# Performance work log

Hardware: AMD Instinct MI355X
Metric: run time of the kernel (lower is better)

Reference implementation:

```python
import jax, jax.numpy as jnp
import numpy as np

ALPHA = 1.0  # init alpha


def setup_inputs() -> dict:
    key = jax.random.key(0)
    X = jax.random.normal(key, (4096, 512), dtype=jnp.float32)
    return {"X": X}


def reference(X):
    # Pairwise squared L2 distances via GEMM expansion:
    # ||x_i - x_j||^2 = ||x_i||^2 + ||x_j||^2 - 2 x_i . x_j
    # (same math as ((X[None]-X[:,None])**2).sum(-1) without the O(N^2 D) blow-up)
    sq = jnp.sum(X * X, axis=1)                      # [N]
    d2 = sq[:, None] + sq[None, :] - 2.0 * (X @ X.T)  # [N, N]
    # track_running_stats=True: sigma^2 = alpha * mean(d2), detached in torch
    sigma_square = ALPHA * jax.lax.stop_gradient(jnp.mean(d2))
    return jnp.exp(-d2 / (2.0 * sigma_square))
```

## Files before the change

kernel.cpp:

```cpp
#include <hip/hip_runtime.h>
#include <cstdint>

typedef unsigned short u16;
typedef unsigned int u32;
typedef __bf16 bf16x8 __attribute__((ext_vector_type(8)));
typedef float f32x4 __attribute__((ext_vector_type(4)));

#define N_ROWS 4096
#define D_COLS 512

__device__ __forceinline__ u16 f2bf(float f) {
    u32 u = __float_as_uint(f);
    u += 0x7fffu + ((u >> 16) & 1u);
    return (u16)(u >> 16);
}

#define GLDS(g, l)                                                            \
    __builtin_amdgcn_global_load_lds(                                         \
        (const __attribute__((address_space(1))) void*)(g),                   \
        (__attribute__((address_space(3))) void*)(l), 16, 0, 0)

__global__ __launch_bounds__(256) void k_prep(const float* __restrict__ X,
                                              u16* __restrict__ Xb,
                                              float* __restrict__ sq,
                                              float* __restrict__ partial) {
    __shared__ float cs[4][512];
    const int tid = threadIdx.x;
    const int w = tid >> 6, l = tid & 63;
    const int row0 = blockIdx.x * 16 + w * 4;
    float csum[8] = {0.f,0.f,0.f,0.f,0.f,0.f,0.f,0.f};
#pragma unroll
    for (int r = 0; r < 4; ++r) {
        const int row = row0 + r;
        const float4* src = (const float4*)(X + (size_t)row * D_COLS);
        float4 f0 = src[l * 2];
        float4 f1 = src[l * 2 + 1];
        float v[8] = {f0.x, f0.y, f0.z, f0.w, f1.x, f1.y, f1.z, f1.w};
        float ss = 0.f;
#pragma unroll
        for (int j = 0; j < 8; ++j) { ss += v[j] * v[j]; csum[j] += v[j]; }
        uint4 st;
        st.x = (u32)f2bf(v[0]) | ((u32)f2bf(v[1]) << 16);
        st.y = (u32)f2bf(v[2]) | ((u32)f2bf(v[3]) << 16);
        st.z = (u32)f2bf(v[4]) | ((u32)f2bf(v[5]) << 16);
        st.w = (u32)f2bf(v[6]) | ((u32)f2bf(v[7]) << 16);
        *(uint4*)(Xb + (size_t)row * D_COLS + l * 8) = st;
#pragma unroll
        for (int m = 32; m > 0; m >>= 1) ss += __shfl_xor(ss, m, 64);
        if (l == 0) sq[row] = ss;
    }
#pragma unroll
    for (int j = 0; j < 8; ++j) cs[w][l * 8 + j] = csum[j];
    __syncthreads();
    for (int d = tid; d < 512; d += 256)
        partial[blockIdx.x * 512 + d] = cs[0][d] + cs[1][d] + cs[2][d] + cs[3][d];
}

__global__ __launch_bounds__(256) void k_sigma(const float* __restrict__ sq,
                                               const float* __restrict__ partial,
                                               float* __restrict__ parts) {
    __shared__ float csm[4][64];
    __shared__ float red[8];
    const int g = blockIdx.x;
    const int t = threadIdx.x;
    const int c = g * 64 + (t & 63);
    const int ch = t >> 6;
    float cssum = 0.f;
#pragma unroll 8
    for (int b = ch * 64; b < ch * 64 + 64; ++b) cssum += partial[b * 512 + c];
    csm[ch][t & 63] = cssum;
    float s1 = sq[g * 512 + t] + sq[g * 512 + 256 + t];
    __syncthreads();
    float s2 = 0.f;
    if (t < 64) {
        float v = csm[0][t] + csm[1][t] + csm[2][t] + csm[3][t];
        s2 = v * v;
    }
#pragma unroll
    for (int m = 32; m > 0; m >>= 1) {
        s1 += __shfl_xor(s1, m, 64);
        s2 += __shfl_xor(s2, m, 64);
    }
    if ((t & 63) == 0) { red[ch] = s1; red[4 + ch] = s2; }
    __syncthreads();
    if (t == 0) {
        parts[g] = red[0] + red[1] + red[2] + red[3];
        parts[8 + g] = red[4];
    }
}

__global__ __launch_bounds__(512, 2) void k_gemm(const u16* __restrict__ Xb,
                                                 const float* __restrict__ sq,
                                                 const float* __restrict__ parts,
                                                 float* __restrict__ out) {
    __shared__ __align__(16) u16 As[3][256 * 32];
    __shared__ __align__(16) u16 Bs[3][256 * 32];
    __shared__ float sqA[256], sqB[256];
    __shared__ float c_sh;

    const int tid = threadIdx.x;
    const int lane = tid & 63;
    const int wid = tid >> 6;
    const int wr = wid >> 2, wc = wid & 3;

    const int bid = blockIdx.x;
    const int xcd = bid & 7, rr = bid >> 3;
    const int by = (xcd >> 2) * 8 + (rr & 7);
    const int bx = (xcd & 3) * 4 + (rr >> 3);
    const int i0 = by * 256, j0 = bx * 256;

    if (tid < 256) sqA[tid] = sq[i0 + tid];
    else           sqB[tid - 256] = sq[j0 + tid - 256];
    if (tid == 0) {
        float S1 = 0.f, S2 = 0.f;
#pragma unroll
        for (int i = 0; i < 8; ++i) { S1 += parts[i]; S2 += parts[8 + i]; }
        const float mean_d2 = 2.f * S1 / (float)N_ROWS
                            - 2.f * S2 / ((float)N_ROWS * (float)N_ROWS);
        c_sh = -1.4426950408889634f / (2.f * mean_d2);
    }

    const int srow = tid >> 2;
    const int sby = (tid & 3) * 16;
    const int ssw = sby ^ ((srow & 3) << 4);
    const char* xb = (const char*)Xb;
    const char* gA0 = xb + (size_t)(i0 + srow) * 1024 + ssw;
    const char* gA1 = xb + (size_t)(i0 + srow + 128) * 1024 + ssw;
    const char* gB0 = xb + (size_t)(j0 + srow) * 1024 + ssw;
    const char* gB1 = xb + (size_t)(j0 + srow + 128) * 1024 + ssw;

#define STAGE(buf, kt)                                                        \
    do {                                                                      \
        GLDS(gA0 + (kt) * 64, (char*)As[buf] + tid * 16);                     \
        GLDS(gA1 + (kt) * 64, (char*)As[buf] + 8192 + tid * 16);              \
        GLDS(gB0 + (kt) * 64, (char*)Bs[buf] + tid * 16);                     \
        GLDS(gB1 + (kt) * 64, (char*)Bs[buf] + 8192 + tid * 16);              \
    } while (0)

    f32x4 acc[8][4];
#pragma unroll
    for (int m = 0; m < 8; ++m)
#pragma unroll
        for (int n = 0; n < 4; ++n) acc[m][n] = (f32x4){0.f, 0.f, 0.f, 0.f};

    const int frow = lane & 15;
    const int klane = lane >> 4;
    const int asw = (klane * 16) ^ ((frow & 3) << 4);
    const int abase = (wr * 128 + frow) * 64 + asw;
    const int bbase = (wc * 64 + frow) * 64 + asw;

    STAGE(0, 0);
    STAGE(1, 1);

    int cb = 0, nb = 2;
    for (int kt = 0; kt < 16; ++kt) {
        if (kt < 15) asm volatile("s_waitcnt vmcnt(4)" ::: "memory");
        else         asm volatile("s_waitcnt vmcnt(0)" ::: "memory");
        asm volatile("s_barrier" ::: "memory");
        if (kt + 2 < 16) STAGE(nb, kt + 2);
        const char* Ab = (const char*)As[cb];
        const char* Bb = (const char*)Bs[cb];
        bf16x8 a[8], b[4];
#pragma unroll
        for (int m = 0; m < 8; ++m) a[m] = *(const bf16x8*)(Ab + abase + m * 1024);
#pragma unroll
        for (int n = 0; n < 4; ++n) b[n] = *(const bf16x8*)(Bb + bbase + n * 1024);
        __builtin_amdgcn_s_setprio(1);
#pragma unroll
        for (int m = 0; m < 8; ++m)
#pragma unroll
            for (int n = 0; n < 4; ++n)
                acc[m][n] = __builtin_amdgcn_mfma_f32_16x16x32_bf16(
                    a[m], b[n], acc[m][n], 0, 0, 0);
        __builtin_amdgcn_s_setprio(0);
        cb = (cb == 2) ? 0 : cb + 1;
        nb = (nb == 2) ? 0 : nb + 1;
    }
#undef STAGE

    const float cval = c_sh;
    const int q = lane >> 4;
#pragma unroll
    for (int m = 0; m < 8; ++m) {
#pragma unroll
        for (int n = 0; n < 4; ++n) {
            const int col = wc * 64 + n * 16 + frow;
            const float sb = sqB[col];
#pragma unroll
            for (int r = 0; r < 4; ++r) {
                const int row = wr * 128 + m * 16 + q * 4 + r;
                const float d2 = sqA[row] + sb - 2.0f * acc[m][n][r];
                out[(size_t)(i0 + row) * N_ROWS + (j0 + col)] = exp2f(cval * d2);
            }
        }
    }
}

extern "C" void kernel_launch(void* const* d_in, const int* in_sizes, int n_in,
                              void* d_out, int out_size, void* d_ws, size_t ws_size,
                              hipStream_t stream) {
    const float* X = (const float*)d_in[0];
    float* out = (float*)d_out;
    char* ws = (char*)d_ws;

    u16*   Xb   = (u16*)ws;
    float* part = (float*)(ws + (4u << 20));
    float* sq   = (float*)(ws + (4u << 20) + (512u << 10));
    float* prt  = (float*)(ws + (4u << 20) + (512u << 10) + (16u << 10));

    hipLaunchKernelGGL(k_prep, dim3(256), dim3(256), 0, stream, X, Xb, sq, part);
    hipLaunchKernelGGL(k_sigma, dim3(8), dim3(256), 0, stream, sq, part, prt);
    hipLaunchKernelGGL(k_gemm, dim3(256), dim3(512), 0, stream, Xb, sq, prt, out);
}
```

Before: 45.83 us.

## Shrink GEMM tile to 128x128 with 4 waves and nontemporal output stores

Changes the fused distance/exp GEMM from 256x256 tiles with 8 waves to 128x128 tiles with 4 waves, launching 1024 blocks with a new XCD-aware block mapping and a revised LDS swizzle. The intent is more blocks per CU and better load balance across CUs. Output stores also become nontemporal to avoid polluting cache with the 64MB result. Smaller tiles cost operand reuse and double global/L2 traffic for the bf16 input.

```diff
diff --git a/kernel.cpp b/kernel.cpp
--- a/kernel.cpp
+++ b/kernel.cpp
@@ -89,28 +89,28 @@
     }
 }
 
-__global__ __launch_bounds__(512, 2) void k_gemm(const u16* __restrict__ Xb,
+__global__ __launch_bounds__(256, 3) void k_gemm(const u16* __restrict__ Xb,
                                                  const float* __restrict__ sq,
                                                  const float* __restrict__ parts,
                                                  float* __restrict__ out) {
-    __shared__ __align__(16) u16 As[3][256 * 32];
-    __shared__ __align__(16) u16 Bs[3][256 * 32];
-    __shared__ float sqA[256], sqB[256];
+    __shared__ __align__(16) u16 As[3][128 * 32];
+    __shared__ __align__(16) u16 Bs[3][128 * 32];
+    __shared__ float sqA[128], sqB[128];
     __shared__ float c_sh;
 
     const int tid = threadIdx.x;
     const int lane = tid & 63;
     const int wid = tid >> 6;
-    const int wr = wid >> 2, wc = wid & 3;
+    const int wr = wid >> 1, wc = wid & 1;
 
     const int bid = blockIdx.x;
     const int xcd = bid & 7, rr = bid >> 3;
-    const int by = (xcd >> 2) * 8 + (rr & 7);
-    const int bx = (xcd & 3) * 4 + (rr >> 3);
-    const int i0 = by * 256, j0 = bx * 256;
-
-    if (tid < 256) sqA[tid] = sq[i0 + tid];
-    else           sqB[tid - 256] = sq[j0 + tid - 256];
+    const int by = (xcd >> 2) * 16 + (rr & 15);
+    const int bx = (xcd & 3) * 8 + (rr >> 4);
+    const int i0 = by * 128, j0 = bx * 128;
+
+    if (tid < 128) sqA[tid] = sq[i0 + tid];
+    else           sqB[tid - 128] = sq[j0 + tid - 128];
     if (tid == 0) {
         float S1 = 0.f, S2 = 0.f;
 #pragma unroll
@@ -120,34 +120,32 @@
         c_sh = -1.4426950408889634f / (2.f * mean_d2);
     }
 
-    const int srow = tid >> 2;
+    const int sr = tid >> 2;
     const int sby = (tid & 3) * 16;
-    const int ssw = sby ^ ((srow & 3) << 4);
+    const int sw0 = sby ^ (((sr >> 1) & 3) << 4);
+    const int sw1 = sby ^ ((((sr + 64) >> 1) & 3) << 4);
     const char* xb = (const char*)Xb;
-    const char* gA0 = xb + (size_t)(i0 + srow) * 1024 + ssw;
-    const char* gA1 = xb + (size_t)(i0 + srow + 128) * 1024 + ssw;
-    const char* gB0 = xb + (size_t)(j0 + srow) * 1024 + ssw;
-    const char* gB1 = xb + (size_t)(j0 + srow + 128) * 1024 + ssw;
+    const char* gA0 = xb + (size_t)(i0 + sr) * 1024 + sw0;
+    const char* gA1 = xb + (size_t)(i0 + sr + 64) * 1024 + sw1;
+    const char* gB0 = xb + (size_t)(j0 + sr) * 1024 + sw0;
+    const char* gB1 = xb + (size_t)(j0 + sr + 64) * 1024 + sw1;
 
 #define STAGE(buf, kt)                                                        \
     do {                                                                      \
         GLDS(gA0 + (kt) * 64, (char*)As[buf] + tid * 16);                     \
-        GLDS(gA1 + (kt) * 64, (char*)As[buf] + 8192 + tid * 16);              \
+        GLDS(gA1 + (kt) * 64, (char*)As[buf] + 4096 + tid * 16);              \
         GLDS(gB0 + (kt) * 64, (char*)Bs[buf] + tid * 16);                     \
-        GLDS(gB1 + (kt) * 64, (char*)Bs[buf] + 8192 + tid * 16);              \
+        GLDS(gB1 + (kt) * 64, (char*)Bs[buf] + 4096 + tid * 16);              \
     } while (0)
 
-    f32x4 acc[8][4];
-#pragma unroll
-    for (int m = 0; m < 8; ++m)
+    f32x4 acc[4][4];
+#pragma unroll
+    for (int m = 0; m < 4; ++m)
 #pragma unroll
         for (int n = 0; n < 4; ++n) acc[m][n] = (f32x4){0.f, 0.f, 0.f, 0.f};
 
     const int frow = lane & 15;
     const int klane = lane >> 4;
-    const int asw = (klane * 16) ^ ((frow & 3) << 4);
-    const int abase = (wr * 128 + frow) * 64 + asw;
-    const int bbase = (wc * 64 + frow) * 64 + asw;
 
     STAGE(0, 0);
     STAGE(1, 1);
@@ -160,14 +158,22 @@
         if (kt + 2 < 16) STAGE(nb, kt + 2);
         const char* Ab = (const char*)As[cb];
         const char* Bb = (const char*)Bs[cb];
-        bf16x8 a[8], b[4];
-#pragma unroll
-        for (int m = 0; m < 8; ++m) a[m] = *(const bf16x8*)(Ab + abase + m * 1024);
-#pragma unroll
-        for (int n = 0; n < 4; ++n) b[n] = *(const bf16x8*)(Bb + bbase + n * 1024);
+        bf16x8 a[4], b[4];
+#pragma unroll
+        for (int m = 0; m < 4; ++m) {
+            const int row = wr * 64 + m * 16 + frow;
+            a[m] = *(const bf16x8*)(Ab + row * 64 +
+                                    ((klane * 16) ^ (((row >> 1) & 3) << 4)));
+        }
+#pragma unroll
+        for (int n = 0; n < 4; ++n) {
+            const int row = wc * 64 + n * 16 + frow;
+            b[n] = *(const bf16x8*)(Bb + row * 64 +
+                                    ((klane * 16) ^ (((row >> 1) & 3) << 4)));
+        }
         __builtin_amdgcn_s_setprio(1);
 #pragma unroll
-        for (int m = 0; m < 8; ++m)
+        for (int m = 0; m < 4; ++m)
 #pragma unroll
             for (int n = 0; n < 4; ++n)
                 acc[m][n] = __builtin_amdgcn_mfma_f32_16x16x32_bf16(
@@ -181,16 +187,18 @@
     const float cval = c_sh;
     const int q = lane >> 4;
 #pragma unroll
-    for (int m = 0; m < 8; ++m) {
+    for (int m = 0; m < 4; ++m) {
 #pragma unroll
         for (int n = 0; n < 4; ++n) {
             const int col = wc * 64 + n * 16 + frow;
             const float sb = sqB[col];
 #pragma unroll
             for (int r = 0; r < 4; ++r) {
-                const int row = wr * 128 + m * 16 + q * 4 + r;
+                const int row = wr * 64 + m * 16 + q * 4 + r;
                 const float d2 = sqA[row] + sb - 2.0f * acc[m][n][r];
-                out[(size_t)(i0 + row) * N_ROWS + (j0 + col)] = exp2f(cval * d2);
+                __builtin_nontemporal_store(
+                    exp2f(cval * d2),
+                    &out[(size_t)(i0 + row) * N_ROWS + (j0 + col)]);
             }
         }
     }
@@ -210,5 +218,5 @@
 
     hipLaunchKernelGGL(k_prep, dim3(256), dim3(256), 0, stream, X, Xb, sq, part);
     hipLaunchKernelGGL(k_sigma, dim3(8), dim3(256), 0, stream, sq, part, prt);
-    hipLaunchKernelGGL(k_gemm, dim3(256), dim3(512), 0, stream, Xb, sq, prt, out);
-}
+    hipLaunchKernelGGL(k_gemm, dim3(1024), dim3(256), 0, stream, Xb, sq, prt, out);
+}
```

New measurement: 53.38 us. 16.5% more time.

## Restructure GEMM main loop into double-buffered BK=64 with interleaved load/MFMA phases

Applied to the files above, without the earlier changes.

Changes the LDS tiling from a triple-buffered 32-wide K step to a double-buffered 64-wide K step with an 8-way XOR swizzle. Each K iteration is split into four phases that interleave partial LDS fragment reads, issues of the next tile's global-to-LDS loads, and MFMA bursts, separated by barriers and explicit waitcnts. The goal is better overlap of memory traffic with matrix math, fewer loop iterations and fewer bank conflicts. The cost is more barriers per iteration and tight vmcnt bookkeeping, which could stall or race if the counts are wrong.

```diff
diff --git a/kernel.cpp b/kernel.cpp
--- a/kernel.cpp
+++ b/kernel.cpp
@@ -89,12 +89,18 @@
     }
 }
 
+#define BAR __builtin_amdgcn_s_barrier()
+#define LGKM0 do { asm volatile("s_waitcnt lgkmcnt(0)" ::: "memory");         \
+                   __builtin_amdgcn_sched_barrier(0); } while (0)
+#define PRIO1 __builtin_amdgcn_s_setprio(1)
+#define PRIO0 __builtin_amdgcn_s_setprio(0)
+
 __global__ __launch_bounds__(512, 2) void k_gemm(const u16* __restrict__ Xb,
                                                  const float* __restrict__ sq,
                                                  const float* __restrict__ parts,
                                                  float* __restrict__ out) {
-    __shared__ __align__(16) u16 As[3][256 * 32];
-    __shared__ __align__(16) u16 Bs[3][256 * 32];
+    __shared__ __align__(16) u16 As[2][256 * 64];
+    __shared__ __align__(16) u16 Bs[2][256 * 64];
     __shared__ float sqA[256], sqB[256];
     __shared__ float c_sh;
 
@@ -119,23 +125,13 @@
                             - 2.f * S2 / ((float)N_ROWS * (float)N_ROWS);
         c_sh = -1.4426950408889634f / (2.f * mean_d2);
     }
-
-    const int srow = tid >> 2;
-    const int sby = (tid & 3) * 16;
-    const int ssw = sby ^ ((srow & 3) << 4);
+    __syncthreads();
+
+    const int strow = tid >> 3;
+    const int sslot = (tid & 7) ^ (strow & 7);
     const char* xb = (const char*)Xb;
-    const char* gA0 = xb + (size_t)(i0 + srow) * 1024 + ssw;
-    const char* gA1 = xb + (size_t)(i0 + srow + 128) * 1024 + ssw;
-    const char* gB0 = xb + (size_t)(j0 + srow) * 1024 + ssw;
-    const char* gB1 = xb + (size_t)(j0 + srow + 128) * 1024 + ssw;
-
-#define STAGE(buf, kt)                                                        \
-    do {                                                                      \
-        GLDS(gA0 + (kt) * 64, (char*)As[buf] + tid * 16);                     \
-        GLDS(gA1 + (kt) * 64, (char*)As[buf] + 8192 + tid * 16);              \
-        GLDS(gB0 + (kt) * 64, (char*)Bs[buf] + tid * 16);                     \
-        GLDS(gB1 + (kt) * 64, (char*)Bs[buf] + 8192 + tid * 16);              \
-    } while (0)
+    const char* gA = xb + (size_t)(i0 + strow) * 1024 + sslot * 16;
+    const char* gB = xb + (size_t)(j0 + strow) * 1024 + sslot * 16;
 
     f32x4 acc[8][4];
 #pragma unroll
@@ -145,38 +141,91 @@
 
     const int frow = lane & 15;
     const int klane = lane >> 4;
-    const int asw = (klane * 16) ^ ((frow & 3) << 4);
-    const int abase = (wr * 128 + frow) * 64 + asw;
-    const int bbase = (wc * 64 + frow) * 64 + asw;
-
-    STAGE(0, 0);
-    STAGE(1, 1);
-
-    int cb = 0, nb = 2;
-    for (int kt = 0; kt < 16; ++kt) {
-        if (kt < 15) asm volatile("s_waitcnt vmcnt(4)" ::: "memory");
-        else         asm volatile("s_waitcnt vmcnt(0)" ::: "memory");
-        asm volatile("s_barrier" ::: "memory");
-        if (kt + 2 < 16) STAGE(nb, kt + 2);
-        const char* Ab = (const char*)As[cb];
-        const char* Bb = (const char*)Bs[cb];
-        bf16x8 a[8], b[4];
-#pragma unroll
-        for (int m = 0; m < 8; ++m) a[m] = *(const bf16x8*)(Ab + abase + m * 1024);
-#pragma unroll
-        for (int n = 0; n < 4; ++n) b[n] = *(const bf16x8*)(Bb + bbase + n * 1024);
-        __builtin_amdgcn_s_setprio(1);
-#pragma unroll
-        for (int m = 0; m < 8; ++m)
-#pragma unroll
-            for (int n = 0; n < 4; ++n)
-                acc[m][n] = __builtin_amdgcn_mfma_f32_16x16x32_bf16(
-                    a[m], b[n], acc[m][n], 0, 0, 0);
-        __builtin_amdgcn_s_setprio(0);
-        cb = (cb == 2) ? 0 : cb + 1;
-        nb = (nb == 2) ? 0 : nb + 1;
-    }
-#undef STAGE
+    const int aoff0 = ((klane ^ (frow & 7)) << 4);
+
+    {
+        char* A0 = (char*)As[0]; char* B0 = (char*)Bs[0];
+        GLDS(gB,               B0 + tid * 16);
+        GLDS(gB + 1 * 65536,   B0 + 1 * 8192 + tid * 16);
+        GLDS(gB + 2 * 65536,   B0 + 2 * 8192 + tid * 16);
+        GLDS(gB + 3 * 65536,   B0 + 3 * 8192 + tid * 16);
+        GLDS(gA,               A0 + tid * 16);
+        GLDS(gA + 2 * 65536,   A0 + 2 * 8192 + tid * 16);
+        GLDS(gA + 1 * 65536,   A0 + 1 * 8192 + tid * 16);
+        GLDS(gA + 3 * 65536,   A0 + 3 * 8192 + tid * 16);
+    }
+    asm volatile("s_waitcnt vmcnt(2)" ::: "memory");
+    BAR;
+
+#define READ_A(mh, ks)                                                        \
+    do {                                                                      \
+        _Pragma("unroll")                                                     \
+        for (int i = 0; i < 4; ++i)                                           \
+            a[i] = *(const bf16x8*)(Ab +                                      \
+                (wr * 128 + (mh) * 64 + i * 16 + frow) * 128 +                \
+                (aoff0 ^ ((ks) * 64)));                                       \
+    } while (0)
+#define READ_B(ks)                                                            \
+    do {                                                                      \
+        _Pragma("unroll")                                                     \
+        for (int n = 0; n < 4; ++n)                                           \
+            b[n] = *(const bf16x8*)(Bb +                                      \
+                (wc * 64 + n * 16 + frow) * 128 +                             \
+                (aoff0 ^ ((ks) * 64)));                                       \
+    } while (0)
+#define MFMA_PH(mh)                                                           \
+    do {                                                                      \
+        _Pragma("unroll")                                                     \
+        for (int i = 0; i < 4; ++i)                                           \
+            _Pragma("unroll")                                                 \
+            for (int n = 0; n < 4; ++n)                                       \
+                acc[(mh) * 4 + i][n] = __builtin_amdgcn_mfma_f32_16x16x32_bf16( \
+                    a[i], b[n], acc[(mh) * 4 + i][n], 0, 0, 0);               \
+    } while (0)
+
+    for (int kt = 0; kt < 8; ++kt) {
+        const int buf = kt & 1;
+        const char* Ab = (const char*)As[buf];
+        const char* Bb = (const char*)Bs[buf];
+        char* AsN = (char*)As[buf ^ 1];
+        char* BsN = (char*)Bs[buf ^ 1];
+        const bool st = kt < 7;
+        const int koff = (kt + 1) * 128;
+        bf16x8 a[4], b[4];
+
+        READ_A(0, 0); READ_B(0);
+        if (st) {
+            GLDS(gB + koff,             BsN + tid * 16);
+            GLDS(gB + 1 * 65536 + koff, BsN + 1 * 8192 + tid * 16);
+        }
+        BAR; LGKM0; PRIO1; MFMA_PH(0); PRIO0;
+        if (st) asm volatile("s_waitcnt vmcnt(2)" ::: "memory");
+        else    asm volatile("s_waitcnt vmcnt(0)" ::: "memory");
+        BAR;
+        READ_A(1, 0);
+        if (st) {
+            GLDS(gB + 2 * 65536 + koff, BsN + 2 * 8192 + tid * 16);
+            GLDS(gB + 3 * 65536 + koff, BsN + 3 * 8192 + tid * 16);
+        }
+        BAR; LGKM0; PRIO1; MFMA_PH(1); PRIO0; BAR;
+        READ_A(0, 1); READ_B(1);
+        if (st) {
+            GLDS(gA + koff,             AsN + tid * 16);
+            GLDS(gA + 2 * 65536 + koff, AsN + 2 * 8192 + tid * 16);
+        }
+        BAR; LGKM0; PRIO1; MFMA_PH(0); PRIO0; BAR;
+        READ_A(1, 1);
+        if (st) {
+            GLDS(gA + 1 * 65536 + koff, AsN + 1 * 8192 + tid * 16);
+            GLDS(gA + 3 * 65536 + koff, AsN + 3 * 8192 + tid * 16);
+        }
+        BAR; LGKM0; PRIO1; MFMA_PH(1); PRIO0;
+        if (st) asm volatile("s_waitcnt vmcnt(2)" ::: "memory");
+        BAR;
+    }
+#undef READ_A
+#undef READ_B
+#undef MFMA_PH
 
     const float cval = c_sh;
     const int q = lane >> 4;
```

Result: no change. 46.45 us (+1.4%).
